# Optimization experiments

Hardware: AMD Instinct MI355X
Metric: run time of the kernel (lower is better)

Reference implementation:

```python
import jax, jax.numpy as jnp
import numpy as np

SEQ_LEN, BATCH, VOCAB, EMB, HID, LAYERS = 128, 128, 10000, 512, 512, 2

def setup_inputs() -> dict:
    key = jax.random.key(0)
    ks = jax.random.split(key, 8)
    k = float(np.sqrt(1.0 / HID))
    inputs = jax.random.randint(ks[0], (SEQ_LEN, BATCH), 0, VOCAB)
    hidden = jnp.zeros((LAYERS, BATCH, HID), dtype=jnp.float32)
    emb = jax.random.uniform(ks[1], (VOCAB, EMB), jnp.float32, -0.1, 0.1)
    W0 = jax.random.uniform(ks[2], (HID, EMB + HID), jnp.float32, -k, k)
    b0 = jax.random.uniform(ks[3], (HID,), jnp.float32, -k, k)
    W1 = jax.random.uniform(ks[4], (HID, 2 * HID), jnp.float32, -k, k)
    b1 = jax.random.uniform(ks[5], (HID,), jnp.float32, -k, k)
    Wout = jax.random.uniform(ks[6], (VOCAB, HID), jnp.float32, -0.1, 0.1)
    bout = jnp.zeros((VOCAB,), dtype=jnp.float32)
    return {"inputs": inputs, "hidden": hidden, "emb": emb, "W0": W0, "b0": b0,
            "W1": W1, "b1": b1, "Wout": Wout, "bout": bout}

def reference(inputs, hidden, emb, W0, b0, W1, b1, Wout, bout):
    # inputs: [S,B] int; hidden: [L,B,H]
    def step(h, tok):
        x = emb[tok]                                              # [B,E]
        h0 = jnp.tanh(jnp.concatenate([x, h[0]], axis=1) @ W0.T + b0)   # [B,H]
        h1 = jnp.tanh(jnp.concatenate([h0, h[1]], axis=1) @ W1.T + b1)  # [B,H]
        logits_t = h1 @ Wout.T + bout                             # [B,V]
        return jnp.stack([h0, h1]), logits_t
    hidden_final, logits = jax.lax.scan(step, hidden, inputs)
    return logits, hidden_final
```

## Files before the change

### kernel.cpp

```cpp
#include <hip/hip_runtime.h>
#include <hip/hip_fp16.h>

typedef _Float16 f16;
typedef _Float16 f16x4 __attribute__((ext_vector_type(4)));
typedef _Float16 f16x8 __attribute__((ext_vector_type(8)));
typedef float f32x4 __attribute__((ext_vector_type(4)));
typedef unsigned u32x2 __attribute__((ext_vector_type(2)));
typedef unsigned u32x4 __attribute__((ext_vector_type(4)));

#define S_LEN 128
#define B_SZ  128
#define VOC   10000
#define VPAD  10240
#define HIDN  512
#define NBLK  64
#define NFLAG 256

#define S0E 5242880
#define S1E 10485760
#define S2E 10747904
#define S3E 10813440
#define S4E 10878976

#define VMCNT(n) do { asm volatile("s_waitcnt vmcnt(" #n ")" ::: "memory"); \
                      __builtin_amdgcn_sched_barrier(0); } while (0)

__device__ __forceinline__ void gload_lds16(const void* g, void* l) {
  __builtin_amdgcn_global_load_lds(
      (const __attribute__((address_space(1))) void*)g,
      (__attribute__((address_space(3))) void*)l, 16, 0, 0);
}

__device__ __forceinline__ f16x8 ld16_dev(const f16* p) {
  u32x4 r;
  asm volatile("global_load_dwordx4 %0, %1, off sc1" : "=v"(r) : "v"(p));
  return __builtin_bit_cast(f16x8, r);
}
__device__ __forceinline__ void cstore8(f16* p, f16x4 v) {
  unsigned long long u = __builtin_bit_cast(unsigned long long, v);
  __hip_atomic_store((unsigned long long*)p, u, __ATOMIC_RELAXED, __HIP_MEMORY_SCOPE_AGENT);
}
__device__ __forceinline__ void stflag_dev(unsigned* p, unsigned v) {
  asm volatile("global_store_dword %0, %1, off sc1" :: "v"(p), "v"(v) : "memory");
}

__device__ __forceinline__ float fast_tanh(float x) {
  float cx = fminf(8.f, fmaxf(-8.f, x));
  float e = __expf(2.f * cx);
  float d = e + 1.f, r;
  asm("v_rcp_f32 %0, %1" : "=v"(r) : "v"(d));
  return (e - 1.f) * r;
}

__global__ __launch_bounds__(256) void convert_all(
    const float* __restrict__ emb, const float* __restrict__ Wout,
    const float* __restrict__ W0, const float* __restrict__ hidden,
    f16* __restrict__ embf16, f16* __restrict__ woutf16,
    f16* __restrict__ w0xf16, f16* __restrict__ h0init, f16* __restrict__ h1init)
{
  const int stride = gridDim.x * 256;
  for (int idx = blockIdx.x * 256 + threadIdx.x; idx < S4E; idx += stride) {
    if (idx < S0E) {
      int r = idx >> 9, c = idx & 511;
      embf16[idx] = (f16)(r < VOC ? emb[(size_t)r * 512 + c] : 0.f);
    } else if (idx < S1E) {
      int i = idx - S0E;
      int r = i >> 9, c = i & 511;
      woutf16[i] = (f16)(r < VOC ? Wout[(size_t)r * 512 + c] : 0.f);
    } else if (idx < S2E) {
      int i = idx - S1E;
      int r = i >> 9, c = i & 511;
      w0xf16[i] = (f16)W0[(size_t)r * 1024 + c];
    } else if (idx < S3E) {
      int i = idx - S2E;
      h0init[i] = (f16)hidden[i];
    } else {
      int i = idx - S3E;
      h1init[i] = (f16)hidden[B_SZ * HIDN + i];
    }
  }
}

template <typename CT>
__global__ __launch_bounds__(512) void gemm_k512(
    const f16* __restrict__ A, const f16* __restrict__ B,
    CT* __restrict__ C, const float* __restrict__ bias,
    int M, int N, int ldc)
{
  __shared__ f16 Asw[256 * 32];
  __shared__ f16 Bsw[128 * 32];
  const int tid  = threadIdx.x;
  const int lane = tid & 63, w = tid >> 6;
  const int wrow = w >> 1, wcol = w & 1;
  int nwg  = gridDim.x * gridDim.y;
  int orig = blockIdx.y * gridDim.x + blockIdx.x;
  int cpx  = nwg >> 3;
  int swz  = (orig & 7) * cpx + (orig >> 3);
  const int m0 = (swz / gridDim.x) * 256, n0 = (swz % gridDim.x) * 128;
  const int rsel = lane & 15, ksl = lane >> 4;

  f32x4 acc[4][4] = {};

  for (int kt = 0; kt < 16; ++kt) {
    __syncthreads();
#pragma unroll
    for (int i = 0; i < 2; ++i) {
      int ac  = i * 8 + w;
      int c   = ac * 64 + lane;
      int row = c >> 2, sp = c & 3;
      int sl  = sp ^ ((row >> 1) & 3);
      gload_lds16(A + (size_t)(m0 + row) * 512 + kt * 32 + sl * 8,
                  &Asw[ac * 512]);
    }
    {
      int c   = w * 64 + lane;
      int row = c >> 2, sp = c & 3;
      int sl  = sp ^ ((row >> 1) & 3);
      gload_lds16(B + (size_t)(n0 + row) * 512 + kt * 32 + sl * 8,
                  &Bsw[w * 512]);
    }
    __syncthreads();

    f16x8 af[4], bf[4];
#pragma unroll
    for (int i = 0; i < 4; ++i) {
      int ar = wrow * 64 + i * 16 + rsel;
      af[i] = *(const f16x8*)&Asw[ar * 32 + ((ksl ^ ((ar >> 1) & 3)) * 8)];
      int br = wcol * 64 + i * 16 + rsel;
      bf[i] = *(const f16x8*)&Bsw[br * 32 + ((ksl ^ ((br >> 1) & 3)) * 8)];
    }
#pragma unroll
    for (int i = 0; i < 4; ++i)
#pragma unroll
      for (int j = 0; j < 4; ++j)
        acc[i][j] = __builtin_amdgcn_mfma_f32_16x16x32_f16(bf[j], af[i], acc[i][j], 0, 0, 0);
  }

#pragma unroll
  for (int i = 0; i < 4; ++i) {
    int row = m0 + wrow * 64 + i * 16 + rsel;
    if (row >= M) continue;
#pragma unroll
    for (int j = 0; j < 4; ++j) {
      int nb = n0 + wcol * 64 + j * 16 + ksl * 4;
      if (nb >= N) continue;
      f32x4 v = acc[i][j];
      if (bias) {
        f32x4 bv = *(const f32x4*)(bias + nb);
        v += bv;
      }
      if constexpr (__is_same(CT, float)) {
        *(f32x4*)&C[(size_t)row * ldc + nb] = v;
      } else {
        f16x4 hv;
#pragma unroll
        for (int q = 0; q < 4; ++q) hv[q] = (f16)v[q];
        *(f16x4*)&C[(size_t)row * ldc + nb] = hv;
      }
    }
  }
}

__global__ __launch_bounds__(256, 1) void rnn_recur(
    const int* __restrict__ tok,
    const float* __restrict__ W0,
    const float* __restrict__ W1,
    const float* __restrict__ b1,
    const f16* __restrict__ P0h,
    f16* __restrict__ h0ring,
    const f16* __restrict__ h1init,
    f16* __restrict__ H1,
    float* __restrict__ outHid,
    unsigned* __restrict__ flags)
{
  __shared__ f16 wlds[3][16 * 512];
  const int tid = threadIdx.x;
  const int lane = tid & 63, w = tid >> 6;
  const int cgI = blockIdx.x & 31, bg = blockIdx.x >> 5;
  const int col0 = cgI * 16;
  const int rowstart = bg * 64 + w * 16;
  const int rsel = lane & 15, ksl = lane >> 4;
  unsigned* gflags = flags + bg * 128;
  const int fidx = cgI * 4 + w;

  for (int it = tid; it < 3 * 16 * 64; it += 256) {
    int s = it >> 10;
    int rem = it & 1023;
    int c = rem >> 6, ks = rem & 63;
    int n = col0 + c;
    const float* srcp;
    if (s == 0)      srcp = W0 + (size_t)n * 1024 + 512 + ks * 8;
    else if (s == 1) srcp = W1 + (size_t)n * 1024 + ks * 8;
    else             srcp = W1 + (size_t)n * 1024 + 512 + ks * 8;
    f16x8 v;
#pragma unroll
    for (int j = 0; j < 8; ++j) v[j] = (f16)srcp[j];
    *(f16x8*)&wlds[s][c * 512 + ((ks ^ (c & 7)) * 8)] = v;
  }
  const f32x4 b1q = *(const f32x4*)(b1 + col0 + ksl * 4);
  __syncthreads();

  const int myrow = rowstart + rsel;
  const size_t hrow = (size_t)myrow * HIDN;
  const int colq = col0 + ksl * 4;
  const unsigned* fptr = gflags + 2 * lane;

  f16x8 hf[16];
  f32x4 part1;

  for (int p = 0; p <= S_LEN + 1; ++p) {
    const bool doH0 = (p <= S_LEN - 1);
    const bool doH1 = (p >= 2);

    if (doH1) {
      f32x4 t = b1q;
#pragma unroll
      for (int kt = 0; kt < 16; ++kt) {
        int ks = kt * 4 + ksl;
        f16x8 b = *(const f16x8*)&wlds[1][rsel * 512 + ((ks ^ (rsel & 7)) * 8)];
        t = __builtin_amdgcn_mfma_f32_16x16x32_f16(b, hf[kt], t, 0, 0, 0);
      }
      part1 = t;
    }
    float pa0, pa1, pa2, pa3;
    if (doH0) {
      int t_ = tok[p * B_SZ + myrow];
      f16x4 pv = *(const f16x4*)&P0h[(size_t)t_ * HIDN + colq];
      pa0 = (float)pv[0]; pa1 = (float)pv[1]; pa2 = (float)pv[2]; pa3 = (float)pv[3];
      asm volatile("" : "+v"(pa0), "+v"(pa1), "+v"(pa2), "+v"(pa3));
    }

    if (p >= 1) {
      const unsigned tgt = (unsigned)p;
      for (;;) {
        u32x2 f;
        asm volatile("global_load_dwordx2 %0, %1, off sc1\n\ts_waitcnt vmcnt(0)"
                     : "=v"(f) : "v"(fptr) : "memory");
        int ok = (f[0] >= tgt) & (f[1] >= tgt);
        if (__all(ok)) break;
      }
    }

    if (p <= S_LEN) {
      const f16* src = h0ring + (size_t)((p - 1) & 3) * B_SZ * HIDN;
#pragma unroll
      for (int kt = 0; kt < 16; ++kt)
        hf[kt] = ld16_dev(src + hrow + kt * 32 + ksl * 8);
    }
    f16x8 h1f[16];
    if (doH1) {
      const f16* h1src = (p == 2) ? h1init : H1 + (size_t)(p - 3) * B_SZ * HIDN;
#pragma unroll
      for (int kt = 0; kt < 16; ++kt)
        h1f[kt] = ld16_dev(h1src + hrow + kt * 32 + ksl * 8);
    }

    float v0, v1, v2, v3;
    if (doH0) {
      if (doH1) { VMCNT(16); } else { VMCNT(0); }
      f32x4 acc0 = {pa0, pa1, pa2, pa3};
#pragma unroll
      for (int kt = 0; kt < 16; ++kt) {
        int ks = kt * 4 + ksl;
        f16x8 b = *(const f16x8*)&wlds[0][rsel * 512 + ((ks ^ (rsel & 7)) * 8)];
        acc0 = __builtin_amdgcn_mfma_f32_16x16x32_f16(b, hf[kt], acc0, 0, 0, 0);
      }
      v0 = fast_tanh(acc0[0]); v1 = fast_tanh(acc0[1]);
      v2 = fast_tanh(acc0[2]); v3 = fast_tanh(acc0[3]);
      f16* dst = h0ring + (size_t)(p & 3) * B_SZ * HIDN;
      f16x4 hv = {(f16)v0, (f16)v1, (f16)v2, (f16)v3};
      cstore8(&dst[hrow + colq], hv);
    }
    if (doH1) {
      if (doH0) { VMCNT(1); } else { VMCNT(0); }
      f32x4 acc1 = part1;
#pragma unroll
      for (int kt = 0; kt < 16; ++kt) {
        int ks = kt * 4 + ksl;
        f16x8 b = *(const f16x8*)&wlds[2][rsel * 512 + ((ks ^ (rsel & 7)) * 8)];
        acc1 = __builtin_amdgcn_mfma_f32_16x16x32_f16(b, h1f[kt], acc1, 0, 0, 0);
      }
      float u0 = fast_tanh(acc1[0]), u1 = fast_tanh(acc1[1]);
      float u2 = fast_tanh(acc1[2]), u3 = fast_tanh(acc1[3]);
      f16* h1dst = H1 + (size_t)(p - 2) * B_SZ * HIDN;
      f16x4 hv = {(f16)u0, (f16)u1, (f16)u2, (f16)u3};
      cstore8(&h1dst[hrow + colq], hv);
      if (p == S_LEN + 1) {
        f32x4 fv = {u0, u1, u2, u3};
        *(f32x4*)&outHid[(size_t)(B_SZ * HIDN) + hrow + colq] = fv;
      }
    }
    if (doH0 && p == S_LEN - 1) {
      f32x4 fv = {v0, v1, v2, v3};
      *(f32x4*)&outHid[hrow + colq] = fv;
    }

    if (p <= S_LEN) {
      VMCNT(0);
      if (lane == 0) stflag_dev(gflags + fidx, (unsigned)(p + 1));
    }
  }
}

extern "C" void kernel_launch(void* const* d_in, const int* in_sizes, int n_in,
                              void* d_out, int out_size, void* d_ws, size_t ws_size,
                              hipStream_t stream) {
  (void)in_sizes; (void)n_in; (void)out_size; (void)ws_size;
  const int*   tok    = (const int*)d_in[0];
  const float* hidden = (const float*)d_in[1];
  const float* emb    = (const float*)d_in[2];
  const float* W0     = (const float*)d_in[3];
  const float* b0     = (const float*)d_in[4];
  const float* W1     = (const float*)d_in[5];
  const float* b1     = (const float*)d_in[6];
  const float* Wout   = (const float*)d_in[7];
  const float* bout   = (const float*)d_in[8];

  char* ws = (char*)d_ws;
  size_t off = 0;
  f16* embf16  = (f16*)(ws + off); off += (size_t)VPAD * 512 * 2;
  f16* woutf16 = (f16*)(ws + off); off += (size_t)VPAD * 512 * 2;
  f16* w0xf16  = (f16*)(ws + off); off += (size_t)512 * 512 * 2;
  f16* P0h     = (f16*)(ws + off); off += (size_t)VOC * 512 * 2;
  f16* H1      = (f16*)(ws + off); off += (size_t)S_LEN * B_SZ * 512 * 2;
  f16* h0ring  = (f16*)(ws + off); off += (size_t)4 * B_SZ * 512 * 2;
  f16* h1init  = (f16*)(ws + off); off += (size_t)B_SZ * 512 * 2;
  unsigned* flags = (unsigned*)(ws + off); off += NFLAG * 4;

  float* outHid = (float*)d_out + (size_t)S_LEN * B_SZ * VOC;

  hipMemsetAsync(flags, 0, NFLAG * 4, stream);

  convert_all<<<2048, 256, 0, stream>>>(
      emb, Wout, W0, hidden, embf16, woutf16, w0xf16,
      h0ring + (size_t)3 * B_SZ * 512, h1init);

  gemm_k512<f16><<<dim3(4, VPAD / 256), 512, 0, stream>>>(
      embf16, w0xf16, P0h, b0, VOC, 512, 512);

  {
    void* args[] = {(void*)&tok, (void*)&W0, (void*)&W1, (void*)&b1, (void*)&P0h,
                    (void*)&h0ring, (void*)&h1init, (void*)&H1, (void*)&outHid, (void*)&flags};
    hipLaunchCooperativeKernel((const void*)rnn_recur, dim3(NBLK), dim3(256), args, 0, stream);
  }

  gemm_k512<float><<<dim3(79, 64), 512, 0, stream>>>(
      H1, woutf16, (float*)d_out, bout, S_LEN * B_SZ, VOC, VOC);
}
```

Before: 1.104 ms.

## Use 32-block recurrence kernel with 32 columns per block

Adds a recurrent kernel variant in which each block owns 32 hidden columns instead of 16, so the grid is 32 cooperative blocks instead of 64. Each block stores 96 KB of fp16 weights in LDS. Each loaded h0/h1 fragment now feeds two MFMAs, which doubles its reuse, and fewer blocks take part in the per-step flag synchronization. The old kernel stays as a fallback, chosen by an occupancy query. In exchange, each block does twice the serial MFMA work per step and the kernel uses far fewer CUs.

```diff
diff --git a/kernel.cpp b/kernel.cpp
--- a/kernel.cpp
+++ b/kernel.cpp
@@ -13,7 +13,6 @@
 #define VOC   10000
 #define VPAD  10240
 #define HIDN  512
-#define NBLK  64
 #define NFLAG 256
 
 #define S0E 5242880
@@ -161,17 +160,172 @@
   }
 }
 
-__global__ __launch_bounds__(256, 1) void rnn_recur(
-    const int* __restrict__ tok,
-    const float* __restrict__ W0,
-    const float* __restrict__ W1,
-    const float* __restrict__ b1,
-    const f16* __restrict__ P0h,
-    f16* __restrict__ h0ring,
-    const f16* __restrict__ h1init,
-    f16* __restrict__ H1,
-    float* __restrict__ outHid,
-    unsigned* __restrict__ flags)
+__global__ __launch_bounds__(256, 1) void rnn_recur32(
+    const int* __restrict__ tok, const float* __restrict__ W0,
+    const float* __restrict__ W1, const float* __restrict__ b1,
+    const f16* __restrict__ P0h, f16* __restrict__ h0ring,
+    const f16* __restrict__ h1init, f16* __restrict__ H1,
+    float* __restrict__ outHid, unsigned* __restrict__ flags)
+{
+  __shared__ f16 wlds[3 * 32 * 512];
+  const int tid = threadIdx.x;
+  const int lane = tid & 63, w = tid >> 6;
+  const int cgI = blockIdx.x & 15, bg = blockIdx.x >> 4;
+  const int col0 = cgI * 32;
+  const int rowstart = bg * 64 + w * 16;
+  const int rsel = lane & 15, ksl = lane >> 4;
+  unsigned* gflags = flags + bg * 64;
+  const int fidx = cgI * 4 + w;
+
+  for (int it = tid; it < 3 * 32 * 64; it += 256) {
+    int s = it >> 11;
+    int rem = it & 2047;
+    int c = rem >> 6, ks = rem & 63;
+    int n = col0 + c;
+    const float* srcp;
+    if (s == 0)      srcp = W0 + (size_t)n * 1024 + 512 + ks * 8;
+    else if (s == 1) srcp = W1 + (size_t)n * 1024 + ks * 8;
+    else             srcp = W1 + (size_t)n * 1024 + 512 + ks * 8;
+    f16x8 v;
+#pragma unroll
+    for (int j = 0; j < 8; ++j) v[j] = (f16)srcp[j];
+    *(f16x8*)&wlds[s * 16384 + c * 512 + ((ks ^ (c & 7)) * 8)] = v;
+  }
+  const f32x4 b1qa = *(const f32x4*)(b1 + col0 + ksl * 4);
+  const f32x4 b1qb = *(const f32x4*)(b1 + col0 + 16 + ksl * 4);
+  __syncthreads();
+
+  const int myrow = rowstart + rsel;
+  const size_t hrow = (size_t)myrow * HIDN;
+  const int ca = col0 + ksl * 4;
+  const int cb = ca + 16;
+  const unsigned* fptr = gflags + lane;
+
+  f16x8 hf[16];
+  f32x4 part1a, part1b;
+
+  for (int p = 0; p <= S_LEN + 1; ++p) {
+    const bool doH0 = (p <= S_LEN - 1);
+    const bool doH1 = (p >= 2);
+
+    if (doH1) {
+      f32x4 ta = b1qa, tb = b1qb;
+#pragma unroll
+      for (int kt = 0; kt < 16; ++kt) {
+        int ks = kt * 4 + ksl;
+        int sw = (ks ^ (rsel & 7)) * 8;
+        f16x8 ba = *(const f16x8*)&wlds[1 * 16384 + rsel * 512 + sw];
+        f16x8 bb = *(const f16x8*)&wlds[1 * 16384 + (16 + rsel) * 512 + sw];
+        ta = __builtin_amdgcn_mfma_f32_16x16x32_f16(ba, hf[kt], ta, 0, 0, 0);
+        tb = __builtin_amdgcn_mfma_f32_16x16x32_f16(bb, hf[kt], tb, 0, 0, 0);
+      }
+      part1a = ta; part1b = tb;
+    }
+    float pa0, pa1, pa2, pa3, pb0, pb1, pb2, pb3;
+    if (doH0) {
+      int t_ = tok[p * B_SZ + myrow];
+      f16x4 pva = *(const f16x4*)&P0h[(size_t)t_ * HIDN + ca];
+      f16x4 pvb = *(const f16x4*)&P0h[(size_t)t_ * HIDN + cb];
+      pa0 = (float)pva[0]; pa1 = (float)pva[1]; pa2 = (float)pva[2]; pa3 = (float)pva[3];
+      pb0 = (float)pvb[0]; pb1 = (float)pvb[1]; pb2 = (float)pvb[2]; pb3 = (float)pvb[3];
+      asm volatile("" : "+v"(pa0), "+v"(pa1), "+v"(pa2), "+v"(pa3),
+                         "+v"(pb0), "+v"(pb1), "+v"(pb2), "+v"(pb3));
+    }
+
+    if (p >= 1) {
+      const unsigned tgt = (unsigned)p;
+      for (;;) {
+        unsigned f;
+        asm volatile("global_load_dword %0, %1, off sc1\n\ts_waitcnt vmcnt(0)"
+                     : "=v"(f) : "v"(fptr) : "memory");
+        if (__all((int)(f >= tgt))) break;
+      }
+    }
+
+    if (p <= S_LEN) {
+      const f16* src = h0ring + (size_t)((p - 1) & 3) * B_SZ * HIDN;
+#pragma unroll
+      for (int kt = 0; kt < 16; ++kt)
+        hf[kt] = ld16_dev(src + hrow + kt * 32 + ksl * 8);
+    }
+    f16x8 h1f[16];
+    if (doH1) {
+      const f16* h1src = (p == 2) ? h1init : H1 + (size_t)(p - 3) * B_SZ * HIDN;
+#pragma unroll
+      for (int kt = 0; kt < 16; ++kt)
+        h1f[kt] = ld16_dev(h1src + hrow + kt * 32 + ksl * 8);
+    }
+
+    float v0, v1, v2, v3, w0_, w1_, w2_, w3_;
+    if (doH0) {
+      if (doH1) { VMCNT(16); } else { VMCNT(0); }
+      f32x4 acc0a = {pa0, pa1, pa2, pa3};
+      f32x4 acc0b = {pb0, pb1, pb2, pb3};
+#pragma unroll
+      for (int kt = 0; kt < 16; ++kt) {
+        int ks = kt * 4 + ksl;
+        int sw = (ks ^ (rsel & 7)) * 8;
+        f16x8 ba = *(const f16x8*)&wlds[0 * 16384 + rsel * 512 + sw];
+        f16x8 bb = *(const f16x8*)&wlds[0 * 16384 + (16 + rsel) * 512 + sw];
+        acc0a = __builtin_amdgcn_mfma_f32_16x16x32_f16(ba, hf[kt], acc0a, 0, 0, 0);
+        acc0b = __builtin_amdgcn_mfma_f32_16x16x32_f16(bb, hf[kt], acc0b, 0, 0, 0);
+      }
+      v0 = fast_tanh(acc0a[0]); v1 = fast_tanh(acc0a[1]);
+      v2 = fast_tanh(acc0a[2]); v3 = fast_tanh(acc0a[3]);
+      w0_ = fast_tanh(acc0b[0]); w1_ = fast_tanh(acc0b[1]);
+      w2_ = fast_tanh(acc0b[2]); w3_ = fast_tanh(acc0b[3]);
+      f16* dst = h0ring + (size_t)(p & 3) * B_SZ * HIDN;
+      f16x4 hva = {(f16)v0, (f16)v1, (f16)v2, (f16)v3};
+      f16x4 hvb = {(f16)w0_, (f16)w1_, (f16)w2_, (f16)w3_};
+      cstore8(&dst[hrow + ca], hva);
+      cstore8(&dst[hrow + cb], hvb);
+    }
+    if (doH1) {
+      if (doH0) { VMCNT(2); } else { VMCNT(0); }
+      f32x4 acc1a = part1a, acc1b = part1b;
+#pragma unroll
+      for (int kt = 0; kt < 16; ++kt) {
+        int ks = kt * 4 + ksl;
+        int sw = (ks ^ (rsel & 7)) * 8;
+        f16x8 ba = *(const f16x8*)&wlds[2 * 16384 + rsel * 512 + sw];
+        f16x8 bb = *(const f16x8*)&wlds[2 * 16384 + (16 + rsel) * 512 + sw];
+        acc1a = __builtin_amdgcn_mfma_f32_16x16x32_f16(ba, h1f[kt], acc1a, 0, 0, 0);
+        acc1b = __builtin_amdgcn_mfma_f32_16x16x32_f16(bb, h1f[kt], acc1b, 0, 0, 0);
+      }
+      float u0 = fast_tanh(acc1a[0]), u1 = fast_tanh(acc1a[1]);
+      float u2 = fast_tanh(acc1a[2]), u3 = fast_tanh(acc1a[3]);
+      float x0 = fast_tanh(acc1b[0]), x1 = fast_tanh(acc1b[1]);
+      float x2 = fast_tanh(acc1b[2]), x3 = fast_tanh(acc1b[3]);
+      f16* h1dst = H1 + (size_t)(p - 2) * B_SZ * HIDN;
+      f16x4 hva = {(f16)u0, (f16)u1, (f16)u2, (f16)u3};
+      f16x4 hvb = {(f16)x0, (f16)x1, (f16)x2, (f16)x3};
+      cstore8(&h1dst[hrow + ca], hva);
+      cstore8(&h1dst[hrow + cb], hvb);
+      if (p == S_LEN + 1) {
+        f32x4 fva = {u0, u1, u2, u3}, fvb = {x0, x1, x2, x3};
+        *(f32x4*)&outHid[(size_t)(B_SZ * HIDN) + hrow + ca] = fva;
+        *(f32x4*)&outHid[(size_t)(B_SZ * HIDN) + hrow + cb] = fvb;
+      }
+    }
+    if (doH0 && p == S_LEN - 1) {
+      f32x4 fva = {v0, v1, v2, v3}, fvb = {w0_, w1_, w2_, w3_};
+      *(f32x4*)&outHid[hrow + ca] = fva;
+      *(f32x4*)&outHid[hrow + cb] = fvb;
+    }
+
+    if (p <= S_LEN) {
+      VMCNT(0);
+      if (lane == 0) stflag_dev(gflags + fidx, (unsigned)(p + 1));
+    }
+  }
+}
+
+__global__ __launch_bounds__(256, 1) void rnn_recur13(
+    const int* __restrict__ tok, const float* __restrict__ W0,
+    const float* __restrict__ W1, const float* __restrict__ b1,
+    const f16* __restrict__ P0h, f16* __restrict__ h0ring,
+    const f16* __restrict__ h1init, f16* __restrict__ H1,
+    float* __restrict__ outHid, unsigned* __restrict__ flags)
 {
   __shared__ f16 wlds[3][16 * 512];
   const int tid = threadIdx.x;
@@ -341,7 +495,13 @@
   {
     void* args[] = {(void*)&tok, (void*)&W0, (void*)&W1, (void*)&b1, (void*)&P0h,
                     (void*)&h0ring, (void*)&h1init, (void*)&H1, (void*)&outHid, (void*)&flags};
-    hipLaunchCooperativeKernel((const void*)rnn_recur, dim3(NBLK), dim3(256), args, 0, stream);
+    int occ32 = 0;
+    (void)hipOccupancyMaxActiveBlocksPerMultiprocessor(&occ32, rnn_recur32, 256, 0);
+    if (occ32 >= 1) {
+      hipLaunchCooperativeKernel((const void*)rnn_recur32, dim3(32), dim3(256), args, 0, stream);
+    } else {
+      hipLaunchCooperativeKernel((const void*)rnn_recur13, dim3(64), dim3(256), args, 0, stream);
+    }
   }
 
   gemm_k512<float><<<dim3(79, 64), 512, 0, stream>>>(
```

Result: slower. 1.265 ms (+14.6%).
